# Kernel optimization log

Measured on AMD Instinct MI355X. Metric: run time of the kernel, lower is better.

Reference implementation:

```python
import jax, jax.numpy as jnp
import numpy as np

N = 100_000   # nodes
E = 1_600_000 # edges
IN = 128
OUT = 64
L = 3         # n_layers


def setup_inputs() -> dict:
    key = jax.random.key(0)
    ks = jax.random.split(key, 4)
    x = jax.random.normal(ks[0], (N, IN), dtype=jnp.float32)
    edge_index = jax.random.randint(ks[1], (2, E), 0, N, dtype=jnp.int64)
    # Glorot-ish init like torch Linear default
    s0 = 1.0 / np.sqrt(IN)
    W0 = jax.random.uniform(ks[2], (IN, OUT), jnp.float32, -s0, s0)
    b0 = jnp.zeros((OUT,), jnp.float32)
    so = 1.0 / np.sqrt(OUT)
    Ws = jax.random.uniform(ks[3], (L - 1, OUT, OUT), jnp.float32, -so, so)
    bs = jnp.zeros((L - 1, OUT), jnp.float32)
    return {"x": x, "edge_index": edge_index, "W0": W0, "b0": b0, "Ws": Ws, "bs": bs}


def _gcn_conv(x, src, dst, norm, W, b):
    # dense transform then degree-normalized scatter-add over edges (incl. self-loops)
    h = x @ W                                  # [N, out]
    msg = h[src] * norm[:, None]               # [E+N, out]
    out = jax.ops.segment_sum(msg, dst, num_segments=N)
    return out + b


def reference(x, edge_index, W0, b0, Ws, bs):
    loops = jnp.arange(N, dtype=edge_index.dtype)
    src = jnp.concatenate([edge_index[0], loops])  # source nodes (x_j)
    dst = jnp.concatenate([edge_index[1], loops])  # aggregation targets
    # symmetric GCN normalization: deg over A+I, norm = d^-1/2[src]*d^-1/2[dst]
    deg = jax.ops.segment_sum(jnp.ones(src.shape, x.dtype), dst, num_segments=N)
    dinv = jnp.where(deg > 0, jax.lax.rsqrt(deg), jnp.zeros((), x.dtype))
    norm = dinv[src] * dinv[dst]

    x_temp = _gcn_conv(x, src, dst, norm, W0, b0)
    h = x_temp
    for i in range(L - 1):  # fixed small layer loop
        h = jax.nn.relu(_gcn_conv(h, src, dst, norm, Ws[i], bs[i]))
    return h + x_temp  # sum_res residual
```

## Files before the change

### kernel.cpp

```cpp
#include <hip/hip_runtime.h>


#define LB 8
#define BKN 256
#define CHUNK 8192
#define CAP 8192
#define CAPCOL (CAP + BKN * 15)

typedef unsigned short ushort_t;
typedef __attribute__((ext_vector_type(8))) short bf16x8;
typedef __attribute__((ext_vector_type(4))) float f32x4;

__device__ __forceinline__ unsigned f2bf(float f) {
    unsigned u = __builtin_bit_cast(unsigned, f);
    return (u + 0x7FFFu + ((u >> 16) & 1u)) >> 16;
}
__device__ __forceinline__ float bf2f(ushort_t h) {
    unsigned u = ((unsigned)h) << 16;
    return __builtin_bit_cast(float, u);
}

__device__ int detect_f64(const int* ei, int E, int* sflag) {
    if (threadIdx.x == 0) *sflag = 0;
    __syncthreads();
    const unsigned* raw = (const unsigned*)ei;
    int dwords = min(2 * E, 4096);
    int any = 0;
    for (int i = threadIdx.x; i < dwords; i += blockDim.x)
        if ((i & 1) && raw[i]) any = 1;
    if (any) atomicOr(sflag, 1);
    __syncthreads();
    return !*sflag;
}

__global__ __launch_bounds__(256) void k_scatter(
        const int* __restrict__ ei, int E,
        int* __restrict__ bucketCursor, unsigned int* __restrict__ packed) {
    __shared__ int hist[512];
    __shared__ int base[512];
    __shared__ int sflag;
    int f64 = detect_f64(ei, E, &sflag);
    int b0 = blockIdx.x * CHUNK;
    int n = min(CHUNK, E - b0);
    for (int i = threadIdx.x; i < 512; i += 256) hist[i] = 0;
    __syncthreads();
    for (int i = threadIdx.x; i < n; i += 256) {
        int e = b0 + i;
        int d = f64 ? ei[2 * (E + e)] : ei[E + e];
        atomicAdd(&hist[d >> LB], 1);
    }
    __syncthreads();
    for (int i = threadIdx.x; i < 512; i += 256) {
        int c = hist[i];
        base[i] = c ? atomicAdd(&bucketCursor[i], c) : 0;
        hist[i] = 0;
    }
    __syncthreads();
    for (int i = threadIdx.x; i < n; i += 256) {
        int e = b0 + i;
        int d = f64 ? ei[2 * (E + e)] : ei[E + e];
        int s = f64 ? ei[2 * e] : ei[e];
        int bk = d >> LB;
        int pos = bk * CAP + base[bk] + atomicAdd(&hist[bk], 1);
        packed[pos] = ((unsigned)s << LB) | (unsigned)(d & (BKN - 1));
    }
}

__global__ __launch_bounds__(256) void k_sort(
        const unsigned int* __restrict__ packed, const int* __restrict__ bucketCursor,
        int* __restrict__ col, int2* __restrict__ rp2, float* __restrict__ dinv,
        ushort_t* __restrict__ hs, int N) {
    __shared__ int hist[BKN];
    __shared__ int s[BKN];
    __shared__ int cur[BKN];
    int tid = threadIdx.x;
    int b = blockIdx.x;
    int start = b * CAP;
    int end = start + bucketCursor[b];
    hist[tid] = 0;
    __syncthreads();
    for (int e = start + tid; e < end; e += 256)
        atomicAdd(&hist[packed[e] & (BKN - 1)], 1);
    __syncthreads();
    int v = hist[tid];
    int pv = (v + 15) & ~15;
    s[tid] = pv;
    __syncthreads();
    for (int off = 1; off < 256; off <<= 1) {
        int x = (tid >= off) ? s[tid - off] : 0;
        __syncthreads();
        if (tid >= off) s[tid] += x;
        __syncthreads();
    }
    int excl = s[tid] - pv;
    int st = b * CAPCOL + excl;
    cur[tid] = st;
    int node = (b << LB) + tid;
    if (node < N) {
        rp2[node] = make_int2(st, st + pv);
        dinv[node] = rsqrtf((float)(v + 1));
        for (int i = v; i < pv; i++) col[st + i] = N;
    }
    if (b == 0 && tid < 64) hs[(size_t)N * 64 + tid] = 0;
    __syncthreads();
    for (int e = start + tid; e < end; e += 256) {
        unsigned pvk = packed[e];
        int pos = atomicAdd(&cur[pvk & (BKN - 1)], 1);
        col[pos] = (int)(pvk >> LB);
    }
}

__global__ __launch_bounds__(256) void k_gemm1(
        const float* __restrict__ A, const float* __restrict__ W,
        const float* __restrict__ dinv, ushort_t* __restrict__ out, int nrows) {
    const int K = 128;
    __shared__ ushort_t sWT[64 * (K + 8)];
    int tid = threadIdx.x;
    for (int i = tid; i < K * 64; i += 256) {
        int n = i & 63, k = i >> 6;
        sWT[n * (K + 8) + k] = (ushort_t)f2bf(W[i]);
    }
    __syncthreads();
    int wave = tid >> 6, lane = tid & 63;
    int quad = lane >> 4, l16 = lane & 15;
    int rowBase = blockIdx.x * 128 + wave * 32;
    f32x4 acc[2][4];
#pragma unroll
    for (int r = 0; r < 2; r++)
#pragma unroll
        for (int c = 0; c < 4; c++) acc[r][c] = (f32x4){0.f, 0.f, 0.f, 0.f};
#pragma unroll
    for (int chunk = 0; chunk < K / 32; chunk++) {
        bf16x8 afr[2];
#pragma unroll
        for (int r = 0; r < 2; r++) {
            int row = rowBase + r * 16 + l16;
            if (row >= nrows) row = nrows - 1;
            const float* ap = A + (size_t)row * K + chunk * 32 + quad * 8;
            float4 v0 = *(const float4*)ap;
            float4 v1 = *(const float4*)(ap + 4);
            bf16x8 a;
            a[0] = (short)f2bf(v0.x); a[1] = (short)f2bf(v0.y);
            a[2] = (short)f2bf(v0.z); a[3] = (short)f2bf(v0.w);
            a[4] = (short)f2bf(v1.x); a[5] = (short)f2bf(v1.y);
            a[6] = (short)f2bf(v1.z); a[7] = (short)f2bf(v1.w);
            afr[r] = a;
        }
#pragma unroll
        for (int c = 0; c < 4; c++) {
            bf16x8 bfr = __builtin_bit_cast(
                bf16x8,
                *(const uint4*)&sWT[(c * 16 + l16) * (K + 8) + chunk * 32 + quad * 8]);
#pragma unroll
            for (int r = 0; r < 2; r++)
                acc[r][c] = __builtin_amdgcn_mfma_f32_16x16x32_bf16(
                    afr[r], bfr, acc[r][c], 0, 0, 0);
        }
    }
#pragma unroll
    for (int r = 0; r < 2; r++)
#pragma unroll
        for (int i = 0; i < 4; i++) {
            int row = rowBase + r * 16 + quad * 4 + i;
            if (row < nrows) {
                float sc = dinv[row];
#pragma unroll
                for (int c = 0; c < 4; c++)
                    out[(size_t)row * 64 + c * 16 + l16] =
                        (ushort_t)f2bf(acc[r][c][i] * sc);
            }
        }
}

__global__ __launch_bounds__(256) void k_gemm64(
        const ushort_t* __restrict__ A, const float* __restrict__ W,
        const float* __restrict__ dinv, ushort_t* __restrict__ out, int nrows) {
    const int K = 64;
    __shared__ ushort_t sWT[64 * (K + 8)];
    int tid = threadIdx.x;
    for (int i = tid; i < K * 64; i += 256) {
        int n = i & 63, k = i >> 6;
        sWT[n * (K + 8) + k] = (ushort_t)f2bf(W[i]);
    }
    __syncthreads();
    int wave = tid >> 6, lane = tid & 63;
    int quad = lane >> 4, l16 = lane & 15;
    int rowBase = blockIdx.x * 128 + wave * 32;
    f32x4 acc[2][4];
#pragma unroll
    for (int r = 0; r < 2; r++)
#pragma unroll
        for (int c = 0; c < 4; c++) acc[r][c] = (f32x4){0.f, 0.f, 0.f, 0.f};
#pragma unroll
    for (int chunk = 0; chunk < K / 32; chunk++) {
        bf16x8 afr[2];
#pragma unroll
        for (int r = 0; r < 2; r++) {
            int row = rowBase + r * 16 + l16;
            if (row >= nrows) row = nrows - 1;
            const ushort_t* ap = A + (size_t)row * K + chunk * 32 + quad * 8;
            afr[r] = __builtin_bit_cast(bf16x8, *(const uint4*)ap);
        }
#pragma unroll
        for (int c = 0; c < 4; c++) {
            bf16x8 bfr = __builtin_bit_cast(
                bf16x8,
                *(const uint4*)&sWT[(c * 16 + l16) * (K + 8) + chunk * 32 + quad * 8]);
#pragma unroll
            for (int r = 0; r < 2; r++)
                acc[r][c] = __builtin_amdgcn_mfma_f32_16x16x32_bf16(
                    afr[r], bfr, acc[r][c], 0, 0, 0);
        }
    }
#pragma unroll
    for (int r = 0; r < 2; r++)
#pragma unroll
        for (int i = 0; i < 4; i++) {
            int row = rowBase + r * 16 + quad * 4 + i;
            if (row < nrows) {
                float sc = dinv[row];
#pragma unroll
                for (int c = 0; c < 4; c++)
                    out[(size_t)row * 64 + c * 16 + l16] =
                        (ushort_t)f2bf(acc[r][c][i] * sc);
            }
        }
}

template <int RELU, int F32OUT>
__global__ __launch_bounds__(256) void k_agg2x(
        const ushort_t* __restrict__ hs, const float* __restrict__ dinv,
        const float* __restrict__ bias, const int* __restrict__ col,
        const int2* __restrict__ rp2, const ushort_t* __restrict__ residb,
        float* __restrict__ outf, ushort_t* __restrict__ outb, int n) {
    int gw = (blockIdx.x * blockDim.x + threadIdx.x) >> 6;
    int lane = threadIdx.x & 63;
    int node0 = gw << 1, node1 = node0 + 1;
    if (node0 >= n) return;
    int2 r0 = rp2[node0];
    int2 r1 = (node1 < n) ? rp2[node1] : make_int2(0, 0);
    float acc0 = bf2f(hs[(size_t)node0 * 64 + lane]);
    float acc1 = (node1 < n) ? bf2f(hs[(size_t)node1 * 64 + lane]) : 0.f;
    int e0 = r0.x, p0 = r0.y;
    int e1 = r1.x, p1 = r1.y;
    while (e0 < p0 || e1 < p1) {
        bool a0 = e0 < p0, a1 = e1 < p1;
        int addr = (lane < 32) ? (e0 + (lane & 15)) : (e1 + (lane & 15));
        int m = col[addr];
        ushort_t u0[16], u1[16];
        if (a0) {
#pragma unroll
            for (int t = 0; t < 16; t++)
                u0[t] = hs[(size_t)__shfl(m, t) * 64 + lane];
        }
        if (a1) {
#pragma unroll
            for (int t = 0; t < 16; t++)
                u1[t] = hs[(size_t)__shfl(m, 32 + t) * 64 + lane];
        }
        if (a0) {
#pragma unroll
            for (int t = 0; t < 16; t += 4)
                acc0 += bf2f(u0[t]) + bf2f(u0[t + 1]) + bf2f(u0[t + 2]) + bf2f(u0[t + 3]);
            e0 += 16;
        }
        if (a1) {
#pragma unroll
            for (int t = 0; t < 16; t += 4)
                acc1 += bf2f(u1[t]) + bf2f(u1[t + 1]) + bf2f(u1[t + 2]) + bf2f(u1[t + 3]);
            e1 += 16;
        }
    }
    float bv = bias[lane];
    {
        float o = dinv[node0] * acc0 + bv;
        if (RELU) o = fmaxf(o, 0.f);
        if (F32OUT) {
            o += bf2f(residb[(size_t)node0 * 64 + lane]);
            outf[(size_t)node0 * 64 + lane] = o;
        } else {
            outb[(size_t)node0 * 64 + lane] = (ushort_t)f2bf(o);
        }
    }
    if (node1 < n) {
        float o = dinv[node1] * acc1 + bv;
        if (RELU) o = fmaxf(o, 0.f);
        if (F32OUT) {
            o += bf2f(residb[(size_t)node1 * 64 + lane]);
            outf[(size_t)node1 * 64 + lane] = o;
        } else {
            outb[(size_t)node1 * 64 + lane] = (ushort_t)f2bf(o);
        }
    }
}

extern "C" void kernel_launch(void* const* d_in, const int* in_sizes, int n_in,
                              void* d_out, int out_size, void* d_ws, size_t ws_size,
                              hipStream_t stream) {
    const float* x  = (const float*)d_in[0];
    const int*   ei = (const int*)d_in[1];
    const float* W0 = (const float*)d_in[2];
    const float* b0 = (const float*)d_in[3];
    const float* Ws = (const float*)d_in[4];
    const float* bs = (const float*)d_in[5];
    float* out = (float*)d_out;

    const int N = in_sizes[0] / 128;
    const int E = in_sizes[1] / 2;
    const int B = (N + BKN - 1) >> LB;

    char* p = (char*)d_ws;
    auto carve = [&](size_t bytes) {
        char* r = p;
        p += (bytes + 255) & ~(size_t)255;
        return r;
    };
    int*      bucketCursor = (int*)carve(512 * 4);
    unsigned* packed       = (unsigned*)carve((size_t)B * CAP * 4);
    int*      col          = (int*)carve(((size_t)B * CAPCOL + 64) * 4);
    int2*     rp2          = (int2*)carve((size_t)N * 8);
    float*    dinv         = (float*)carve((size_t)N * 4);
    ushort_t* hs           = (ushort_t*)carve((size_t)(N + 1) * 64 * 2);
    ushort_t* xtb          = (ushort_t*)carve((size_t)N * 64 * 2);
    ushort_t* hb           = (ushort_t*)carve((size_t)N * 64 * 2);

    hipMemsetAsync(bucketCursor, 0, 512 * 4, stream);

    k_scatter<<<(E + CHUNK - 1) / CHUNK, 256, 0, stream>>>(ei, E, bucketCursor, packed);
    k_sort<<<B, 256, 0, stream>>>(packed, bucketCursor, col, rp2, dinv, hs, N);

    int gb = (N + 127) / 128;
    int ablocks = (N + 7) / 8;

    k_gemm1<<<gb, 256, 0, stream>>>(x, W0, dinv, hs, N);
    k_agg2x<0, 0><<<ablocks, 256, 0, stream>>>(hs, dinv, b0, col, rp2,
                                               nullptr, nullptr, xtb, N);
    k_gemm64<<<gb, 256, 0, stream>>>(xtb, Ws, dinv, hs, N);
    k_agg2x<1, 0><<<ablocks, 256, 0, stream>>>(hs, dinv, bs, col, rp2,
                                               nullptr, nullptr, hb, N);
    k_gemm64<<<gb, 256, 0, stream>>>(hb, Ws + 64 * 64, dinv, hs, N);
    k_agg2x<1, 1><<<ablocks, 256, 0, stream>>>(hs, dinv, bs + 64, col, rp2,
                                               xtb, out, nullptr, N);
}
```

Measured before the change: 305.6 us.

## Gather four edges per wavefront with 8-byte loads and pad rows to 8

Rewrites the aggregation kernel so each wavefront processes one node, with four 16-lane groups each gathering a different neighbor row using 8-byte (4×bf16) loads, then reduces across groups with shuffles. Column padding per node drops from multiples of 16 to multiples of 8, which cuts the dummy-edge gathers for low-degree nodes and adds a half-tile tail path. The aim is fewer, wider memory transactions and less wasted padding work. The cost is cross-lane reductions and one node per wave instead of two.

```diff
diff --git a/kernel.cpp b/kernel.cpp
--- a/kernel.cpp
+++ b/kernel.cpp
@@ -5,7 +5,8 @@
 #define BKN 256
 #define CHUNK 8192
 #define CAP 8192
-#define CAPCOL (CAP + BKN * 15)
+#define PADS 7
+#define CAPCOL (CAP + BKN * PADS)
 
 typedef unsigned short ushort_t;
 typedef __attribute__((ext_vector_type(8))) short bf16x8;
@@ -18,6 +19,12 @@
 __device__ __forceinline__ float bf2f(ushort_t h) {
     unsigned u = ((unsigned)h) << 16;
     return __builtin_bit_cast(float, u);
+}
+__device__ __forceinline__ float bflo(unsigned u) {
+    return __builtin_bit_cast(float, u << 16);
+}
+__device__ __forceinline__ float bfhi(unsigned u) {
+    return __builtin_bit_cast(float, u & 0xFFFF0000u);
 }
 
 __device__ int detect_f64(const int* ei, int E, int* sflag) {
@@ -83,7 +90,7 @@
         atomicAdd(&hist[packed[e] & (BKN - 1)], 1);
     __syncthreads();
     int v = hist[tid];
-    int pv = (v + 15) & ~15;
+    int pv = (v + PADS) & ~PADS;
     s[tid] = pv;
     __syncthreads();
     for (int off = 1; off < 256; off <<= 1) {
@@ -228,68 +235,68 @@
 }
 
 template <int RELU, int F32OUT>
-__global__ __launch_bounds__(256) void k_agg2x(
+__global__ __launch_bounds__(256) void k_agg4e(
         const ushort_t* __restrict__ hs, const float* __restrict__ dinv,
         const float* __restrict__ bias, const int* __restrict__ col,
         const int2* __restrict__ rp2, const ushort_t* __restrict__ residb,
         float* __restrict__ outf, ushort_t* __restrict__ outb, int n) {
-    int gw = (blockIdx.x * blockDim.x + threadIdx.x) >> 6;
+    int node = (int)((blockIdx.x * blockDim.x + threadIdx.x) >> 6);
+    if (node >= n) return;
     int lane = threadIdx.x & 63;
-    int node0 = gw << 1, node1 = node0 + 1;
-    if (node0 >= n) return;
-    int2 r0 = rp2[node0];
-    int2 r1 = (node1 < n) ? rp2[node1] : make_int2(0, 0);
-    float acc0 = bf2f(hs[(size_t)node0 * 64 + lane]);
-    float acc1 = (node1 < n) ? bf2f(hs[(size_t)node1 * 64 + lane]) : 0.f;
-    int e0 = r0.x, p0 = r0.y;
-    int e1 = r1.x, p1 = r1.y;
-    while (e0 < p0 || e1 < p1) {
-        bool a0 = e0 < p0, a1 = e1 < p1;
-        int addr = (lane < 32) ? (e0 + (lane & 15)) : (e1 + (lane & 15));
-        int m = col[addr];
-        ushort_t u0[16], u1[16];
-        if (a0) {
-#pragma unroll
-            for (int t = 0; t < 16; t++)
-                u0[t] = hs[(size_t)__shfl(m, t) * 64 + lane];
-        }
-        if (a1) {
-#pragma unroll
-            for (int t = 0; t < 16; t++)
-                u1[t] = hs[(size_t)__shfl(m, 32 + t) * 64 + lane];
-        }
-        if (a0) {
-#pragma unroll
-            for (int t = 0; t < 16; t += 4)
-                acc0 += bf2f(u0[t]) + bf2f(u0[t + 1]) + bf2f(u0[t + 2]) + bf2f(u0[t + 3]);
-            e0 += 16;
-        }
-        if (a1) {
-#pragma unroll
-            for (int t = 0; t < 16; t += 4)
-                acc1 += bf2f(u1[t]) + bf2f(u1[t + 1]) + bf2f(u1[t + 2]) + bf2f(u1[t + 3]);
-            e1 += 16;
-        }
-    }
-    float bv = bias[lane];
-    {
-        float o = dinv[node0] * acc0 + bv;
-        if (RELU) o = fmaxf(o, 0.f);
+    int g = lane >> 4;
+    int c4 = lane & 15;
+    const ushort_t* hrow = hs + (size_t)c4 * 4;
+    int2 r = rp2[node];
+    int e = r.x, p = r.y;
+    uint2 us = *(const uint2*)(hs + (size_t)node * 64 + c4 * 4);
+    float a0 = 0.f, a1 = 0.f, a2 = 0.f, a3 = 0.f;
+
+#define GLOAD(T, O)                                                         \
+    int m##T = __shfl(idx, g + (O));                                        \
+    uint2 u##T = *(const uint2*)(hrow + (size_t)m##T * 64);
+#define GACC(T)                                                             \
+    a0 += bflo(u##T.x); a1 += bfhi(u##T.x);                                 \
+    a2 += bflo(u##T.y); a3 += bfhi(u##T.y);
+
+    for (; e + 16 <= p; e += 16) {
+        int idx = col[e + c4];
+        GLOAD(0, 0) GLOAD(1, 4) GLOAD(2, 8) GLOAD(3, 12)
+        GACC(0) GACC(1) GACC(2) GACC(3)
+    }
+    if (e < p) {
+        int idx = col[e + c4];
+        GLOAD(0, 0) GLOAD(1, 4)
+        GACC(0) GACC(1)
+    }
+#undef GLOAD
+#undef GACC
+
+    a0 += __shfl_xor(a0, 16); a0 += __shfl_xor(a0, 32);
+    a1 += __shfl_xor(a1, 16); a1 += __shfl_xor(a1, 32);
+    a2 += __shfl_xor(a2, 16); a2 += __shfl_xor(a2, 32);
+    a3 += __shfl_xor(a3, 16); a3 += __shfl_xor(a3, 32);
+
+    if (lane < 16) {
+        a0 += bflo(us.x); a1 += bfhi(us.x);
+        a2 += bflo(us.y); a3 += bfhi(us.y);
+        float sc = dinv[node];
+        float4 bv = *(const float4*)(bias + c4 * 4);
+        float o0 = sc * a0 + bv.x, o1 = sc * a1 + bv.y;
+        float o2 = sc * a2 + bv.z, o3 = sc * a3 + bv.w;
+        if (RELU) {
+            o0 = fmaxf(o0, 0.f); o1 = fmaxf(o1, 0.f);
+            o2 = fmaxf(o2, 0.f); o3 = fmaxf(o3, 0.f);
+        }
         if (F32OUT) {
-            o += bf2f(residb[(size_t)node0 * 64 + lane]);
-            outf[(size_t)node0 * 64 + lane] = o;
+            uint2 rb = *(const uint2*)(residb + (size_t)node * 64 + c4 * 4);
+            o0 += bflo(rb.x); o1 += bfhi(rb.x);
+            o2 += bflo(rb.y); o3 += bfhi(rb.y);
+            *(float4*)(outf + (size_t)node * 64 + c4 * 4) =
+                make_float4(o0, o1, o2, o3);
         } else {
-            outb[(size_t)node0 * 64 + lane] = (ushort_t)f2bf(o);
-        }
-    }
-    if (node1 < n) {
-        float o = dinv[node1] * acc1 + bv;
-        if (RELU) o = fmaxf(o, 0.f);
-        if (F32OUT) {
-            o += bf2f(residb[(size_t)node1 * 64 + lane]);
-            outf[(size_t)node1 * 64 + lane] = o;
-        } else {
-            outb[(size_t)node1 * 64 + lane] = (ushort_t)f2bf(o);
+            unsigned w0 = f2bf(o0) | (f2bf(o1) << 16);
+            unsigned w1 = f2bf(o2) | (f2bf(o3) << 16);
+            *(uint2*)(outb + (size_t)node * 64 + c4 * 4) = make_uint2(w0, w1);
         }
     }
 }
@@ -330,15 +337,15 @@
     k_sort<<<B, 256, 0, stream>>>(packed, bucketCursor, col, rp2, dinv, hs, N);
 
     int gb = (N + 127) / 128;
-    int ablocks = (N + 7) / 8;
+    int ablocks = (N + 3) / 4;
 
     k_gemm1<<<gb, 256, 0, stream>>>(x, W0, dinv, hs, N);
-    k_agg2x<0, 0><<<ablocks, 256, 0, stream>>>(hs, dinv, b0, col, rp2,
+    k_agg4e<0, 0><<<ablocks, 256, 0, stream>>>(hs, dinv, b0, col, rp2,
                                                nullptr, nullptr, xtb, N);
     k_gemm64<<<gb, 256, 0, stream>>>(xtb, Ws, dinv, hs, N);
-    k_agg2x<1, 0><<<ablocks, 256, 0, stream>>>(hs, dinv, bs, col, rp2,
+    k_agg4e<1, 0><<<ablocks, 256, 0, stream>>>(hs, dinv, bs, col, rp2,
                                                nullptr, nullptr, hb, N);
     k_gemm64<<<gb, 256, 0, stream>>>(hb, Ws + 64 * 64, dinv, hs, N);
-    k_agg2x<1, 1><<<ablocks, 256, 0, stream>>>(hs, dinv, bs + 64, col, rp2,
+    k_agg4e<1, 1><<<ablocks, 256, 0, stream>>>(hs, dinv, bs + 64, col, rp2,
                                                xtb, out, nullptr, N);
 }
```

Result: no change. 301.8 us (-1.2%).
